# Kernel tuning notes

Measured on AMD Instinct MI355X. Metric: run time of the kernel, lower is better.

Reference implementation:

```python
import jax, jax.numpy as jnp
import numpy as np

B, H, W, CIN, C, L = 2, 512, 512, 64, 64, 4
TAU = 1.0


def _conv3x3(x, w):
    # NHWC input, HWIO kernel, SAME zero padding, stride 1 (SignalConv2D corr=True)
    return jax.lax.conv_general_dilated(
        x, w, window_strides=(1, 1), padding='SAME',
        dimension_numbers=('NHWC', 'HWIO', 'NHWC'))


def setup_inputs() -> dict:
    key = jax.random.key(0)
    ks = jax.random.split(key, 10)
    return {
        'x0': jax.random.normal(ks[0], (B, H, W, CIN), jnp.float32),
        'spa_mask': jax.random.uniform(ks[1], (B, H, W, 1), jnp.float32),
        'gumbel_u': jax.random.uniform(ks[2], (1, L, 2, C), jnp.float32),
        'ch_mask': jax.random.uniform(ks[3], (1, L, 2, C), jnp.float32),
        'w0': jax.random.normal(ks[4], (3, 3, CIN, C), jnp.float32) * 0.05,
        'w1': jax.random.normal(ks[5], (3, 3, C, C), jnp.float32) * 0.05,
        'w2': jax.random.normal(ks[6], (3, 3, C, C), jnp.float32) * 0.05,
        'w3': jax.random.normal(ks[7], (3, 3, C, C), jnp.float32) * 0.05,
        'w_collect': jax.random.normal(ks[8], (L * C, C), jnp.float32) * 0.05,
        'b_collect': jnp.zeros((C,), jnp.float32),
    }


def reference(x0, spa_mask, gumbel_u, ch_mask, w0, w1, w2, w3, w_collect, b_collect):
    # Gumbel-softmax channel routing mask over the {dense, sparse} axis (axis=2)
    g = -jnp.log(-jnp.log(jnp.clip(gumbel_u, 1e-10, 1.0)))
    ch = jax.nn.softmax((ch_mask + g) / TAU, axis=2)  # (1, L, 2, C)

    ws = [w0, w1, w2, w3]
    out_feats = []
    fea = x0
    for i in range(L):
        cd = ch[:, i, 0, :][:, None, None, :]  # dense-channel mask  (1,1,1,C)
        cs = ch[:, i, 1, :][:, None, None, :]  # sparse-channel mask (1,1,1,C)
        if i == 0:
            fea = _conv3x3(fea, ws[0])
            fea = fea * cs * spa_mask + fea * cd
        else:
            cdp = ch[:, i - 1, 0, :][:, None, None, :]
            csp = ch[:, i - 1, 1, :][:, None, None, :]
            fea_d = _conv3x3(fea * cdp, ws[i])
            fea_s = _conv3x3(fea * csp, ws[i])
            fea = (fea_d * cs * spa_mask + fea_d * cd
                   + fea_s * cs * spa_mask + fea_s * cd * spa_mask)
        fea = jax.nn.relu(fea)
        out_feats.append(fea)

    cat = jnp.concatenate(out_feats, axis=-1)  # (B, H, W, L*C)
    # 1x1 stride-1 Conv2DTranspose == pointwise linear + bias
    out = jnp.einsum('bhwi,io->bhwo', cat, w_collect) + b_collect
    return out, ch
```

## Files before the change

kernel.cpp:

```cpp
#include <hip/hip_runtime.h>
#include <hip/hip_fp16.h>

#define BB 2
#define HH 512
#define WW 512
#define CC 64
#define PW 514
#define PIMG (514*514)

typedef _Float16 f16;
typedef _Float16 f16x8 __attribute__((ext_vector_type(8)));
typedef float f32x4 __attribute__((ext_vector_type(4)));

static __device__ __forceinline__ f16x8 zero_f16x8() {
    f16x8 z = {(f16)0,(f16)0,(f16)0,(f16)0,(f16)0,(f16)0,(f16)0,(f16)0};
    return z;
}

__global__ void k_prep_ch(const float* __restrict__ gum, const float* __restrict__ chm,
                          float* __restrict__ ws_ch, float* __restrict__ out_ch) {
    int t = threadIdx.x;
    int l = t >> 6, c = t & 63;
    float u0 = gum[(l*2+0)*64+c], u1 = gum[(l*2+1)*64+c];
    u0 = fminf(fmaxf(u0, 1e-10f), 1.0f);
    u1 = fminf(fmaxf(u1, 1e-10f), 1.0f);
    float a0 = chm[(l*2+0)*64+c] - logf(-logf(u0));
    float a1 = chm[(l*2+1)*64+c] - logf(-logf(u1));
    float m = fmaxf(a0, a1);
    float e0 = expf(a0-m), e1 = expf(a1-m);
    float s = e0 + e1;
    float c0 = e0/s, c1 = e1/s;
    ws_ch[(l*2+0)*64+c] = c0;  ws_ch[(l*2+1)*64+c] = c1;
    out_ch[(l*2+0)*64+c] = c0; out_ch[(l*2+1)*64+c] = c1;
}

__global__ void k_pack(const float* __restrict__ w0, const float* __restrict__ w1,
                       const float* __restrict__ w2, const float* __restrict__ w3,
                       const float* __restrict__ wc, const float* __restrict__ ch,
                       f16* __restrict__ bpk0, f16* __restrict__ bpkL, f16* __restrict__ wcpk) {
    int idx = blockIdx.x * 256 + threadIdx.x;
    if (idx < 36864) {
        int j = idx & 7, lane = (idx>>3)&63, nb = (idx>>9)&3, kb = idx>>11;
        int k = kb*32 + (lane>>4)*8 + j;
        int tap = k>>6, ci = k&63;
        int co = nb*16 + (lane&15);
        bpk0[idx] = (f16)w0[(tap*64+ci)*64+co];
    } else if (idx < 36864 + 221184) {
        int i2 = idx - 36864;
        int l = i2 / 73728;
        int r = i2 % 73728;
        int j = r&7, lane=(r>>3)&63, nb=(r>>9)&7, kb=r>>12;
        int k = kb*32 + (lane>>4)*8 + j;
        int tap = k>>6, ci = k&63;
        int copr = nb*16 + (lane&15);
        int co = copr & 63;
        const float* w = (l==0)? w1 : (l==1)? w2 : w3;
        float scale = (copr < 64) ? ch[(l*2+0)*64+ci] : ch[(l*2+1)*64+ci];
        bpkL[i2] = (f16)(w[(tap*64+ci)*64+co] * scale);
    } else if (idx < 36864 + 221184 + 16384) {
        int i3 = idx - (36864 + 221184);
        int j=i3&7, lane=(i3>>3)&63, nb=(i3>>9)&3, kb=(i3>>11)&1, l=i3>>12;
        int k = kb*32 + (lane>>4)*8 + j;
        int n = nb*16 + (lane&15);
        wcpk[i3] = (f16)wc[(l*64+k)*64+n];
    }
}

__global__ void k_cvt_pad(const float* __restrict__ x, f16* __restrict__ y) {
    int idx = blockIdx.x*256 + threadIdx.x;
    const int TOT = 2*PIMG*8;
    if (idx >= TOT) return;
    int c8 = idx & 7;
    int pxl = idx >> 3;
    int b = pxl / PIMG, r = pxl % PIMG;
    int hp = r / PW, wp = r % PW;
    f16x8 o;
    if (hp >= 1 && hp <= 512 && wp >= 1 && wp <= 512) {
        const float* p = x + (((size_t)(b*HH + hp-1)*WW + (wp-1))*CC + c8*8);
        float4 v0 = *(const float4*)p, v1 = *(const float4*)(p+4);
        o[0]=(f16)v0.x; o[1]=(f16)v0.y; o[2]=(f16)v0.z; o[3]=(f16)v0.w;
        o[4]=(f16)v1.x; o[5]=(f16)v1.y; o[6]=(f16)v1.z; o[7]=(f16)v1.w;
    } else o = zero_f16x8();
    *(f16x8*)(y + (size_t)pxl*64 + c8*8) = o;
}

__global__ void k_guard(f16* __restrict__ buf) {
    int idx = blockIdx.x*256 + threadIdx.x;
    const int TOT = 2*2052*8;
    if (idx >= TOT) return;
    int c8 = idx & 7, g = idx >> 3;
    int b = g / 2052, r = g % 2052;
    int hp, wp;
    if      (r < 514)  { hp = 0;        wp = r; }
    else if (r < 1028) { hp = 513;      wp = r-514; }
    else if (r < 1540) { hp = r-1027;   wp = 0; }
    else               { hp = r-1539;   wp = 513; }
    *(f16x8*)(buf + ((size_t)(b*PW+hp)*PW + wp)*64 + c8*8) = zero_f16x8();
}

template<int MODE>
__global__ __launch_bounds__(256, 2) void k_conv(const f16* __restrict__ in, f16* __restrict__ out,
        const f16* __restrict__ bpk, const float* __restrict__ ch_l,
        const float* __restrict__ spa) {
    constexpr int NBT = (MODE==0) ? 4 : 8;
    constexpr int NF  = (MODE==0) ? 2 : 4;
    __shared__ f16 smem[4*136*64];
    const int wt = blockIdx.x, hb = blockIdx.y, b = blockIdx.z;
    const int h0 = hb*2;
    const int tid = threadIdx.x, lane = tid & 63, wid = tid >> 6;
    const int px0 = wt*128;
    const int sub  = lane & 7;
    const int srel = lane >> 3;

    #pragma unroll
    for (int jj = 0; jj < 17; ++jj) {
        int j = jj*4 + wid;
        int r = j / 17, i = j % 17;
        int s = i*8 + srel;
        int cblk = sub ^ (s & 7);
        const f16* src = in + ((size_t)(b*PW + h0 + r)*PW + (px0 + s))*64 + cblk*8;
        __builtin_amdgcn_global_load_lds(
            (const __attribute__((address_space(1))) uint32_t*)src,
            (__attribute__((address_space(3))) uint32_t*)
                ((char*)smem + r*17408 + i*1024),
            16, 0, 0);
    }
    __syncthreads();

    const int wr = wid >> 1, wn = wid & 1;
    const int lrow = lane & 15, q = lane >> 4;
    const char* smw = (const char*)smem + wr*17408;

    int sb[8][3], po[2][3];
    #pragma unroll
    for (int dxi = 0; dxi < 3; ++dxi) {
        int m7 = (lrow + dxi) & 7;
        po[0][dxi] = ((q)     ^ m7) * 16;
        po[1][dxi] = ((4 + q) ^ m7) * 16;
        #pragma unroll
        for (int mf = 0; mf < 8; ++mf)
            sb[mf][dxi] = (mf*16 + lrow + dxi) * 128;
    }

    f32x4 acc[8][NF];
    #pragma unroll
    for (int i=0;i<8;i++)
        #pragma unroll
        for (int j=0;j<NF;j++) { f32x4 z = {0.f,0.f,0.f,0.f}; acc[i][j] = z; }

    int nbIdx[4];
    nbIdx[0]=wn*2; nbIdx[1]=wn*2+1; nbIdx[2]=wn*2+4; nbIdx[3]=wn*2+5;

    const f16* blane = bpk + (size_t)lane*8;

    f16x8 acur[8], anxt[8], bcur[NF], bnxt[NF];
    #pragma unroll
    for (int nf=0; nf<NF; ++nf)
        bcur[nf] = *reinterpret_cast<const f16x8*>(blane + (size_t)nbIdx[nf]*512);
    #pragma unroll
    for (int mf=0; mf<8; ++mf)
        acur[mf] = *(const f16x8*)(smw + sb[mf][0] + po[0][0]);

    #pragma unroll
    for (int kb = 0; kb < 18; ++kb) {
        if (kb < 17) {
            const int kn = kb + 1;
            const int rn = kn/6, dxin = (kn%6)/2, halfn = kn & 1;
            #pragma unroll
            for (int nf=0; nf<NF; ++nf)
                bnxt[nf] = *reinterpret_cast<const f16x8*>(blane + (size_t)(kn*NBT + nbIdx[nf])*512);
            #pragma unroll
            for (int mf=0; mf<8; ++mf)
                anxt[mf] = *(const f16x8*)(smw + rn*17408 + sb[mf][dxin] + po[halfn][dxin]);
        }
        __builtin_amdgcn_s_setprio(1);
        #pragma unroll
        for (int nf=0; nf<NF; ++nf) {
            #pragma unroll
            for (int mf=0; mf<8; ++mf)
                acc[mf][nf] = __builtin_amdgcn_mfma_f32_16x16x32_f16(acur[mf], bcur[nf], acc[mf][nf], 0,0,0);
        }
        __builtin_amdgcn_s_setprio(0);
        #pragma unroll
        for (int nf=0; nf<NF; ++nf) bcur[nf] = bnxt[nf];
        #pragma unroll
        for (int mf=0; mf<8; ++mf) acur[mf] = anxt[mf];
    }

    const float* cd = ch_l;
    const float* cs = ch_l + 64;
    const int h = h0 + wr;
    const size_t sparow = (size_t)(b*HH + h)*WW;
    const size_t outrow = (size_t)(b*PW + h + 1)*PW + 1;
    #pragma unroll
    for (int mf=0; mf<8; ++mf) {
        const int pixb = mf*16 + q*4;
        float4 sp4 = *(const float4*)(spa + sparow + px0 + pixb);
        float sp[4] = {sp4.x, sp4.y, sp4.z, sp4.w};
        #pragma unroll
        for (int nf2=0; nf2<2; ++nf2) {
            int co = wn*32 + nf2*16 + lrow;
            float vcd = cd[co], vcs = cs[co];
            #pragma unroll
            for (int r=0; r<4; ++r) {
                float v;
                if (MODE==0) v = acc[mf][nf2][r] * (vcs*sp[r] + vcd);
                else         v = acc[mf][nf2][r] * (vcs*sp[r] + vcd) + acc[mf][nf2+2][r] * sp[r];
                v = fmaxf(v, 0.f);
                out[(outrow + px0 + pixb + r)*64 + co] = (f16)v;
            }
        }
    }
}

__global__ __launch_bounds__(256) void k_collect_all(
        const f16* __restrict__ f0, const f16* __restrict__ f1,
        const f16* __restrict__ f2, const f16* __restrict__ f3,
        const f16* __restrict__ wcpk, const float* __restrict__ bias,
        float* __restrict__ out) {
    const int wt = blockIdx.x, h = blockIdx.y, b = blockIdx.z;
    const int tid = threadIdx.x;
    const int lane = tid & 63, wid = tid >> 6;
    const int lrow = lane & 15, lk = (lane>>4)*8;
    const size_t inrow  = (size_t)(b*PW + h + 1)*PW + 1;
    const size_t outrow = (size_t)(b*HH + h)*WW;
    const int px0 = wt*256 + wid*64;

    const f16* feas[4] = {f0, f1, f2, f3};

    f32x4 acc[4][4];
    #pragma unroll
    for (int i=0;i<4;i++)
        #pragma unroll
        for (int j=0;j<4;j++) { f32x4 z = {0.f,0.f,0.f,0.f}; acc[i][j] = z; }

    #pragma unroll
    for (int kb=0; kb<8; ++kb) {
        const f16* fl = feas[kb>>1];
        f16x8 a[4];
        #pragma unroll
        for (int mf=0; mf<4; ++mf)
            a[mf] = *reinterpret_cast<const f16x8*>(fl + (inrow + px0 + mf*16 + lrow)*64 + (kb&1)*32 + lk);
        #pragma unroll
        for (int nf=0; nf<4; ++nf) {
            f16x8 bb = *reinterpret_cast<const f16x8*>(wcpk + ((size_t)(kb*4 + nf)*64 + lane)*8);
            #pragma unroll
            for (int mf=0; mf<4; ++mf)
                acc[mf][nf] = __builtin_amdgcn_mfma_f32_16x16x32_f16(a[mf], bb, acc[mf][nf], 0,0,0);
        }
    }
    #pragma unroll
    for (int mf=0; mf<4; ++mf) {
        const int pixb = px0 + mf*16 + (lane>>4)*4;
        #pragma unroll
        for (int nf=0; nf<4; ++nf) {
            int co = nf*16 + lrow;
            float bv = bias[co];
            #pragma unroll
            for (int r=0;r<4;++r)
                out[(outrow + pixb + r)*CC + co] = acc[mf][nf][r] + bv;
        }
    }
}

template<bool FIRST>
__global__ __launch_bounds__(256) void k_collect(const f16* __restrict__ fea,
        const f16* __restrict__ wcpk_l, const float* __restrict__ bias,
        float* __restrict__ out) {
    const int wt = blockIdx.x, h = blockIdx.y, b = blockIdx.z;
    const int tid = threadIdx.x;
    const int lane = tid & 63, wid = tid >> 6;
    const int lrow = lane & 15, lk = (lane>>4)*8;
    const size_t inrow  = (size_t)(b*PW + h + 1)*PW + 1;
    const size_t outrow = (size_t)(b*HH + h)*WW;
    const int px0 = wt*64 + wid*16;

    f32x4 acc[4];
    #pragma unroll
    for (int j=0;j<4;j++) { f32x4 z = {0.f,0.f,0.f,0.f}; acc[j] = z; }

    #pragma unroll
    for (int kb=0; kb<2; ++kb) {
        f16x8 a = *reinterpret_cast<const f16x8*>(fea + (inrow + px0 + lrow)*64 + kb*32 + lk);
        #pragma unroll
        for (int nf=0; nf<4; ++nf) {
            f16x8 bb = *reinterpret_cast<const f16x8*>(wcpk_l + ((size_t)(kb*4 + nf)*64 + lane)*8);
            acc[nf] = __builtin_amdgcn_mfma_f32_16x16x32_f16(a, bb, acc[nf], 0,0,0);
        }
    }
    #pragma unroll
    for (int nf=0; nf<4; ++nf) {
        int co = nf*16 + lrow;
        #pragma unroll
        for (int r=0;r<4;++r) {
            int pix = px0 + (lane>>4)*4 + r;
            size_t o = (outrow + pix)*CC + co;
            float v = acc[nf][r];
            if (FIRST) v += bias[co];
            else       v += out[o];
            out[o] = v;
        }
    }
}

extern "C" void kernel_launch(void* const* d_in, const int* in_sizes, int n_in,
                              void* d_out, int out_size, void* d_ws, size_t ws_size,
                              hipStream_t stream) {
    const float* x0  = (const float*)d_in[0];
    const float* spa = (const float*)d_in[1];
    const float* gum = (const float*)d_in[2];
    const float* chm = (const float*)d_in[3];
    const float* w0  = (const float*)d_in[4];
    const float* w1  = (const float*)d_in[5];
    const float* w2  = (const float*)d_in[6];
    const float* w3  = (const float*)d_in[7];
    const float* wc  = (const float*)d_in[8];
    const float* bias= (const float*)d_in[9];
    float* out = (float*)d_out;

    char* ws = (char*)d_ws;
    const size_t WBASE = (1u<<20);
    const size_t FB = 67699712ull;
    const size_t NEED_A = WBASE + 4*FB;
    const size_t NEED_B = WBASE + 2*FB;
    if (ws_size < NEED_B) return;

    float* ws_ch = (float*)ws;
    f16* bpk0 = (f16*)(ws + 4096);
    f16* bpkL = (f16*)(ws + 4096 + 73728);
    f16* wcpk = (f16*)(ws + 4096 + 73728 + 442368);

    k_prep_ch<<<1, 256, 0, stream>>>(gum, chm, ws_ch, out + 33554432);
    k_pack<<<1072, 256, 0, stream>>>(w0, w1, w2, w3, wc, ws_ch, bpk0, bpkL, wcpk);

    const int CVT_GRID = (2*PIMG*8 + 255)/256;
    dim3 gcv(4, 256, 2);
    dim3 gca(2, 512, 2);
    dim3 gcf(8, 512, 2);

    if (ws_size >= NEED_A) {
        f16* R0 = (f16*)(ws + WBASE);
        f16* R1 = (f16*)(ws + WBASE + FB);
        f16* R2 = (f16*)(ws + WBASE + 2*FB);
        f16* R3 = (f16*)(ws + WBASE + 3*FB);
        k_guard<<<129, 256, 0, stream>>>(R1);
        k_guard<<<129, 256, 0, stream>>>(R2);
        k_guard<<<129, 256, 0, stream>>>(R3);
        k_cvt_pad<<<CVT_GRID, 256, 0, stream>>>(x0, R0);
        k_conv<0><<<gcv, 256, 0, stream>>>(R0, R1, bpk0,          ws_ch + 0,   spa);
        k_conv<1><<<gcv, 256, 0, stream>>>(R1, R2, bpkL + 0,      ws_ch + 128, spa);
        k_conv<1><<<gcv, 256, 0, stream>>>(R2, R3, bpkL + 73728,  ws_ch + 256, spa);
        k_conv<1><<<gcv, 256, 0, stream>>>(R3, R0, bpkL + 147456, ws_ch + 384, spa);
        k_collect_all<<<gca, 256, 0, stream>>>(R1, R2, R3, R0, wcpk, bias, out);
    } else {
        f16* P0 = (f16*)(ws + WBASE);
        f16* P1 = (f16*)(ws + WBASE + FB);
        k_guard<<<129, 256, 0, stream>>>(P0);
        k_guard<<<129, 256, 0, stream>>>(P1);
        k_cvt_pad<<<CVT_GRID, 256, 0, stream>>>(x0, P0);
        k_conv<0><<<gcv, 256, 0, stream>>>(P0, P1, bpk0,          ws_ch + 0,   spa);
        k_collect<true ><<<gcf, 256, 0, stream>>>(P1, wcpk + 0,     bias, out);
        k_conv<1><<<gcv, 256, 0, stream>>>(P1, P0, bpkL + 0,      ws_ch + 128, spa);
        k_collect<false><<<gcf, 256, 0, stream>>>(P0, wcpk + 4096,  bias, out);
        k_conv<1><<<gcv, 256, 0, stream>>>(P0, P1, bpkL + 73728,  ws_ch + 256, spa);
        k_collect<false><<<gcf, 256, 0, stream>>>(P1, wcpk + 8192,  bias, out);
        k_conv<1><<<gcv, 256, 0, stream>>>(P1, P0, bpkL + 147456, ws_ch + 384, spa);
        k_collect<false><<<gcf, 256, 0, stream>>>(P0, wcpk + 12288, bias, out);
    }
}
```

Before: 380.2 us.

## Split conv tile LDS fill into two phases overlapped with early MFMA work

The conv kernel now waits only on the first two input rows before starting MFMAs. The remaining two rows are issued as asynchronous global-to-LDS loads and synchronised at k-block 5, just before they are first read. This hides part of the tile load latency behind compute, at the cost of an extra barrier inside the main loop. The cvt_pad kernel switches to a 3D grid that removes the integer divides and uses nontemporal loads, and collect_all writes its output with nontemporal stores to reduce cache pollution.

```diff
diff --git a/kernel.cpp b/kernel.cpp
--- a/kernel.cpp
+++ b/kernel.cpp
@@ -67,21 +67,19 @@
 }
 
 __global__ void k_cvt_pad(const float* __restrict__ x, f16* __restrict__ y) {
-    int idx = blockIdx.x*256 + threadIdx.x;
-    const int TOT = 2*PIMG*8;
-    if (idx >= TOT) return;
-    int c8 = idx & 7;
-    int pxl = idx >> 3;
-    int b = pxl / PIMG, r = pxl % PIMG;
-    int hp = r / PW, wp = r % PW;
+    const int hp = blockIdx.y, b = blockIdx.z;
+    int u = blockIdx.x*256 + threadIdx.x;
+    if (u >= PW*8) return;
+    int wp = u >> 3, c8 = u & 7;
     f16x8 o;
     if (hp >= 1 && hp <= 512 && wp >= 1 && wp <= 512) {
-        const float* p = x + (((size_t)(b*HH + hp-1)*WW + (wp-1))*CC + c8*8);
-        float4 v0 = *(const float4*)p, v1 = *(const float4*)(p+4);
-        o[0]=(f16)v0.x; o[1]=(f16)v0.y; o[2]=(f16)v0.z; o[3]=(f16)v0.w;
-        o[4]=(f16)v1.x; o[5]=(f16)v1.y; o[6]=(f16)v1.z; o[7]=(f16)v1.w;
+        const f32x4* p = (const f32x4*)(x + (((size_t)(b*HH + hp-1)*WW + (wp-1))*CC + c8*8));
+        f32x4 v0 = __builtin_nontemporal_load(p);
+        f32x4 v1 = __builtin_nontemporal_load(p+1);
+        o[0]=(f16)v0[0]; o[1]=(f16)v0[1]; o[2]=(f16)v0[2]; o[3]=(f16)v0[3];
+        o[4]=(f16)v1[0]; o[5]=(f16)v1[1]; o[6]=(f16)v1[2]; o[7]=(f16)v1[3];
     } else o = zero_f16x8();
-    *(f16x8*)(y + (size_t)pxl*64 + c8*8) = o;
+    *(f16x8*)(y + ((size_t)(b*PW + hp)*PW + wp)*64 + c8*8) = o;
 }
 
 __global__ void k_guard(f16* __restrict__ buf) {
@@ -113,19 +111,36 @@
     const int srel = lane >> 3;
 
     #pragma unroll
-    for (int jj = 0; jj < 17; ++jj) {
+    for (int jj = 0; jj < 9; ++jj) {
         int j = jj*4 + wid;
-        int r = j / 17, i = j % 17;
-        int s = i*8 + srel;
-        int cblk = sub ^ (s & 7);
-        const f16* src = in + ((size_t)(b*PW + h0 + r)*PW + (px0 + s))*64 + cblk*8;
-        __builtin_amdgcn_global_load_lds(
-            (const __attribute__((address_space(1))) uint32_t*)src,
-            (__attribute__((address_space(3))) uint32_t*)
-                ((char*)smem + r*17408 + i*1024),
-            16, 0, 0);
+        if (j < 34) {
+            int r = j / 17, i = j % 17;
+            int s = i*8 + srel;
+            int cblk = sub ^ (s & 7);
+            const f16* src = in + ((size_t)(b*PW + h0 + r)*PW + (px0 + s))*64 + cblk*8;
+            __builtin_amdgcn_global_load_lds(
+                (const __attribute__((address_space(1))) uint32_t*)src,
+                (__attribute__((address_space(3))) uint32_t*)
+                    ((char*)smem + r*17408 + i*1024),
+                16, 0, 0);
+        }
     }
     __syncthreads();
+    #pragma unroll
+    for (int jj = 0; jj < 9; ++jj) {
+        int j = 34 + jj*4 + wid;
+        if (j < 68) {
+            int r = j / 17, i = j % 17;
+            int s = i*8 + srel;
+            int cblk = sub ^ (s & 7);
+            const f16* src = in + ((size_t)(b*PW + h0 + r)*PW + (px0 + s))*64 + cblk*8;
+            __builtin_amdgcn_global_load_lds(
+                (const __attribute__((address_space(1))) uint32_t*)src,
+                (__attribute__((address_space(3))) uint32_t*)
+                    ((char*)smem + r*17408 + i*1024),
+                16, 0, 0);
+        }
+    }
 
     const int wr = wid >> 1, wn = wid & 1;
     const int lrow = lane & 15, q = lane >> 4;
@@ -163,6 +178,7 @@
 
     #pragma unroll
     for (int kb = 0; kb < 18; ++kb) {
+        if (kb == 5) __syncthreads();
         if (kb < 17) {
             const int kn = kb + 1;
             const int rn = kn/6, dxin = (kn%6)/2, halfn = kn & 1;
@@ -195,8 +211,8 @@
     #pragma unroll
     for (int mf=0; mf<8; ++mf) {
         const int pixb = mf*16 + q*4;
-        float4 sp4 = *(const float4*)(spa + sparow + px0 + pixb);
-        float sp[4] = {sp4.x, sp4.y, sp4.z, sp4.w};
+        f32x4 sp4 = *(const f32x4*)(spa + sparow + px0 + pixb);
+        float sp[4] = {sp4[0], sp4[1], sp4[2], sp4[3]};
         #pragma unroll
         for (int nf2=0; nf2<2; ++nf2) {
             int co = wn*32 + nf2*16 + lrow;
@@ -258,7 +274,8 @@
             float bv = bias[co];
             #pragma unroll
             for (int r=0;r<4;++r)
-                out[(outrow + pixb + r)*CC + co] = acc[mf][nf][r] + bv;
+                __builtin_nontemporal_store(acc[mf][nf][r] + bv,
+                                            &out[(outrow + pixb + r)*CC + co]);
         }
     }
 }
@@ -333,7 +350,7 @@
     k_prep_ch<<<1, 256, 0, stream>>>(gum, chm, ws_ch, out + 33554432);
     k_pack<<<1072, 256, 0, stream>>>(w0, w1, w2, w3, wc, ws_ch, bpk0, bpkL, wcpk);
 
-    const int CVT_GRID = (2*PIMG*8 + 255)/256;
+    dim3 gct(17, 514, 2);
     dim3 gcv(4, 256, 2);
     dim3 gca(2, 512, 2);
     dim3 gcf(8, 512, 2);
@@ -346,7 +363,7 @@
         k_guard<<<129, 256, 0, stream>>>(R1);
         k_guard<<<129, 256, 0, stream>>>(R2);
         k_guard<<<129, 256, 0, stream>>>(R3);
-        k_cvt_pad<<<CVT_GRID, 256, 0, stream>>>(x0, R0);
+        k_cvt_pad<<<gct, 256, 0, stream>>>(x0, R0);
         k_conv<0><<<gcv, 256, 0, stream>>>(R0, R1, bpk0,          ws_ch + 0,   spa);
         k_conv<1><<<gcv, 256, 0, stream>>>(R1, R2, bpkL + 0,      ws_ch + 128, spa);
         k_conv<1><<<gcv, 256, 0, stream>>>(R2, R3, bpkL + 73728,  ws_ch + 256, spa);
@@ -357,7 +374,7 @@
         f16* P1 = (f16*)(ws + WBASE + FB);
         k_guard<<<129, 256, 0, stream>>>(P0);
         k_guard<<<129, 256, 0, stream>>>(P1);
-        k_cvt_pad<<<CVT_GRID, 256, 0, stream>>>(x0, P0);
+        k_cvt_pad<<<gct, 256, 0, stream>>>(x0, P0);
         k_conv<0><<<gcv, 256, 0, stream>>>(P0, P1, bpk0,          ws_ch + 0,   spa);
         k_collect<true ><<<gcf, 256, 0, stream>>>(P1, wcpk + 0,     bias, out);
         k_conv<1><<<gcv, 256, 0, stream>>>(P1, P0, bpkL + 0,      ws_ch + 128, spa);
```

After: 375.1 us. About the same (-1.4%).
